# Kernel tuning notes

Measured on AMD Instinct MI355X. Metric: run time of the kernel, lower is better.

The kernel has to match this reference:

```python
import jax, jax.numpy as jnp
import numpy as np

V, D, L, H, T_BLK, DFF = 50257, 768, 12, 12, 1024, 4096
DK = D // H
LN_EPS = 1e-5


def setup_inputs() -> dict:
    key = jax.random.key(0)
    ks = jax.random.split(key, 16)
    s = 0.02
    inp = {
        "idx": jax.random.randint(ks[0], (2, 1024), 0, V),
        "tok_emb": jax.random.normal(ks[1], (V, D), jnp.float32) * s,
        "pos_emb": jax.random.normal(ks[2], (1, T_BLK, D), jnp.float32) * s,
        "ln1_w": jnp.ones((L, D), jnp.float32),
        "ln1_b": jnp.zeros((L, D), jnp.float32),
        "qkv_w": jax.random.normal(ks[3], (L, 3 * D, D), jnp.float32) * s,
        "qkv_b": jnp.zeros((L, 3 * D), jnp.float32),
        "proj_w": jax.random.normal(ks[4], (L, D, D), jnp.float32) * s,
        "proj_b": jnp.zeros((L, D), jnp.float32),
        "ln2_w": jnp.ones((L, D), jnp.float32),
        "ln2_b": jnp.zeros((L, D), jnp.float32),
        "ff1_w": jax.random.normal(ks[5], (L, DFF, D), jnp.float32) * s,
        "ff1_b": jnp.zeros((L, DFF), jnp.float32),
        "ff2_w": jax.random.normal(ks[6], (L, D, DFF), jnp.float32) * s,
        "ff2_b": jnp.zeros((L, D), jnp.float32),
        "lnf_w": jnp.ones((D,), jnp.float32),
        "lnf_b": jnp.zeros((D,), jnp.float32),
        "head_w": jax.random.normal(ks[7], (V, D), jnp.float32) * s,
    }
    return inp


def _layernorm(x, w, b):
    mu = jnp.mean(x, axis=-1, keepdims=True)
    var = jnp.var(x, axis=-1, keepdims=True)
    return (x - mu) * jax.lax.rsqrt(var + LN_EPS) * w + b


def _gpt_forward(idx, tok_emb, pos_emb, ln1_w, ln1_b, qkv_w, qkv_b, proj_w, proj_b,
                 ln2_w, ln2_b, ff1_w, ff1_b, ff2_w, ff2_b, lnf_w, lnf_b, head_w):
    B, T = idx.shape
    x = tok_emb[idx] + pos_emb[:, :T, :]  # [B,T,D]
    mask = jnp.tril(jnp.ones((T, T), bool))  # causal
    scale = 1.0 / np.sqrt(DK)

    def step(x, p):
        l1w, l1b, qw, qb, pw, pb, l2w, l2b, f1w, f1b, f2w, f2b = p
        h = _layernorm(x, l1w, l1b)
        qkv = h @ qw.T + qb  # [B,T,3D]
        q, k, v = jnp.split(qkv, 3, axis=-1)
        q = q.reshape(B, T, H, DK).transpose(0, 2, 1, 3)  # [B,H,T,DK]
        k = k.reshape(B, T, H, DK).transpose(0, 2, 1, 3)
        v = v.reshape(B, T, H, DK).transpose(0, 2, 1, 3)
        att = jnp.einsum('bhtd,bhsd->bhts', q, k) * scale
        att = jnp.where(mask, att, -jnp.inf)
        att = jax.nn.softmax(att, axis=-1)
        y = jnp.einsum('bhts,bhsd->bhtd', att, v)
        y = y.transpose(0, 2, 1, 3).reshape(B, T, D)
        x = x + y @ pw.T + pb
        h2 = _layernorm(x, l2w, l2b)
        ff = jax.nn.gelu(h2 @ f1w.T + f1b, approximate=False) @ f2w.T + f2b
        return x + ff, None

    params = (ln1_w, ln1_b, qkv_w, qkv_b, proj_w, proj_b,
              ln2_w, ln2_b, ff1_w, ff1_b, ff2_w, ff2_b)
    x, _ = jax.lax.scan(step, x, params)
    x = _layernorm(x, lnf_w, lnf_b)
    return x @ head_w.T  # [B,T,V] logits


def reference(idx, tok_emb, pos_emb, ln1_w, ln1_b, qkv_w, qkv_b, proj_w, proj_b,
              ln2_w, ln2_b, ff1_w, ff1_b, ff2_w, ff2_b, lnf_w, lnf_b, head_w):
    return _gpt_forward(idx, tok_emb, pos_emb, ln1_w, ln1_b, qkv_w, qkv_b, proj_w,
                        proj_b, ln2_w, ln2_b, ff1_w, ff1_b, ff2_w, ff2_b,
                        lnf_w, lnf_b, head_w)
```

## Files before the change

kernel.cpp:

```cpp
#include <hip/hip_runtime.h>
#include <hip/hip_bf16.h>
#include <math.h>

#define Dm 768
#define Tt 1024
#define Bb 2
#define Hh 12
#define DFF 4096
#define Ll 12
#define Vv 50257
#define ROWS (Bb*Tt)
#define LN_EPS 1e-5f

typedef unsigned int uint;
typedef unsigned short ushort;
typedef float f32x4 __attribute__((ext_vector_type(4)));
typedef short bf16x8 __attribute__((ext_vector_type(8)));
typedef ushort us8 __attribute__((ext_vector_type(8)));

__device__ __forceinline__ ushort f2bf(float f) {
  uint u = __builtin_bit_cast(uint, f);
  u += 0x7FFFu + ((u >> 16) & 1u);
  return (ushort)(u >> 16);
}

#define GLL(gp, lp)                                                          \
  __builtin_amdgcn_global_load_lds(                                          \
      (const __attribute__((address_space(1))) uint*)(gp),                   \
      (__attribute__((address_space(3))) uint*)(lp), 16, 0, 0)

#define MF(a, b, c) __builtin_amdgcn_mfma_f32_16x16x32_bf16(a, b, c, 0, 0, 0)

__global__ __launch_bounds__(256) void embed_ln(
    const int* __restrict__ idx, const float* __restrict__ tok,
    const float* __restrict__ pos, const float* __restrict__ w,
    const float* __restrict__ b, float* __restrict__ x,
    ushort* __restrict__ out) {
  const int row = blockIdx.x;
  const int t = row & (Tt - 1);
  const int tid = threadIdx.x;
  const float* tsrc = tok + (size_t)idx[row] * Dm;
  const float* psrc = pos + (size_t)t * Dm;
  float v[3];
  float sum = 0.f, sq = 0.f;
#pragma unroll
  for (int i = 0; i < 3; i++) {
    const int d = tid + i * 256;
    v[i] = tsrc[d] + psrc[d];
    x[(size_t)row * Dm + d] = v[i];
    sum += v[i]; sq += v[i] * v[i];
  }
#pragma unroll
  for (int off = 32; off > 0; off >>= 1) {
    sum += __shfl_xor(sum, off);
    sq  += __shfl_xor(sq, off);
  }
  __shared__ float red[8];
  const int wid = tid >> 6, lane = tid & 63;
  if (lane == 0) { red[wid] = sum; red[wid + 4] = sq; }
  __syncthreads();
  sum = red[0] + red[1] + red[2] + red[3];
  sq  = red[4] + red[5] + red[6] + red[7];
  const float mu = sum * (1.f / Dm);
  const float var = sq * (1.f / Dm) - mu * mu;
  const float rstd = rsqrtf(var + LN_EPS);
  ushort* dst = out + (size_t)row * Dm;
#pragma unroll
  for (int i = 0; i < 3; i++) {
    const int d = tid + i * 256;
    dst[d] = f2bf((v[i] - mu) * rstd * w[d] + b[d]);
  }
}

__global__ __launch_bounds__(192) void red_ln(
    const float* __restrict__ part, int nsk, const float* __restrict__ bias,
    float* __restrict__ x, const float* __restrict__ w,
    const float* __restrict__ b, ushort* __restrict__ out) {
  const int row = blockIdx.x;
  const int tid = threadIdx.x;
  const size_t o4 = (size_t)row * 192 + tid;
  float4 xv = ((const float4*)x)[o4];
  const float4 b4 = ((const float4*)bias)[tid];
  xv.x += b4.x; xv.y += b4.y; xv.z += b4.z; xv.w += b4.w;
  for (int k = 0; k < nsk; k++) {
    const float4 p = ((const float4*)part)[(size_t)k * ROWS * 192 + o4];
    xv.x += p.x; xv.y += p.y; xv.z += p.z; xv.w += p.w;
  }
  ((float4*)x)[o4] = xv;
  float sum = xv.x + xv.y + xv.z + xv.w;
  float sq = xv.x * xv.x + xv.y * xv.y + xv.z * xv.z + xv.w * xv.w;
#pragma unroll
  for (int off = 32; off > 0; off >>= 1) {
    sum += __shfl_xor(sum, off);
    sq  += __shfl_xor(sq, off);
  }
  __shared__ float red[6];
  const int wid = tid >> 6, lane = tid & 63;
  if (lane == 0) { red[wid] = sum; red[wid + 3] = sq; }
  __syncthreads();
  sum = red[0] + red[1] + red[2];
  sq  = red[3] + red[4] + red[5];
  const float mu = sum * (1.f / Dm);
  const float var = sq * (1.f / Dm) - mu * mu;
  const float rstd = rsqrtf(var + LN_EPS);
  const float4 w4 = ((const float4*)w)[tid];
  const float4 bb4 = ((const float4*)b)[tid];
  ushort4 o;
  o.x = f2bf((xv.x - mu) * rstd * w4.x + bb4.x);
  o.y = f2bf((xv.y - mu) * rstd * w4.y + bb4.y);
  o.z = f2bf((xv.z - mu) * rstd * w4.z + bb4.z);
  o.w = f2bf((xv.w - mu) * rstd * w4.w + bb4.w);
  ((ushort4*)out)[o4] = o;
}

#define C1 5308416
#define C2 7077888
#define C3 16515072
#define C4 25952256
#define NALL4 35601600

__global__ __launch_bounds__(256) void convert_all(
    const float* __restrict__ q, const float* __restrict__ p,
    const float* __restrict__ f1, const float* __restrict__ f2,
    const float* __restrict__ hd, ushort* __restrict__ wb) {
  const int stride = gridDim.x * 256;
  for (int i = blockIdx.x * 256 + threadIdx.x; i < NALL4; i += stride) {
    const float* s; int j;
    if (i < C1) { s = q; j = i; }
    else if (i < C2) { s = p; j = i - C1; }
    else if (i < C3) { s = f1; j = i - C2; }
    else if (i < C4) { s = f2; j = i - C3; }
    else { s = hd; j = i - C4; }
    const float4 v = ((const float4*)s)[j];
    ushort4 o;
    o.x = f2bf(v.x); o.y = f2bf(v.y); o.z = f2bf(v.z); o.w = f2bf(v.w);
    ((ushort4*)wb)[i] = o;
  }
}

#define EPI_QKV 0
#define EPI_PART 1
#define EPI_BIAS_GELU 2
#define EPI_NONE 3

template <int EPI>
__global__ __launch_bounds__(256) void gemm_mfma(
    const ushort* __restrict__ A, const ushort* __restrict__ B,
    const float* __restrict__ bias, void* __restrict__ Cv,
    void* __restrict__ Cv2, int Kloop, int Kstr, int Nloc, int ldC) {
  __shared__ char lds[32768];
  const int tid = threadIdx.x;
  const int l = tid & 63;
  const int wid = __builtin_amdgcn_readfirstlane(tid >> 6);
  const int wr = wid >> 1, wc = wid & 1;
  const int m0 = blockIdx.y * 128;
  const int n0 = blockIdx.x * 128;
  const int z = (EPI == EPI_PART) ? blockIdx.z : 0;
  if (EPI == EPI_PART) { A += (size_t)z * Kloop; B += (size_t)z * Kloop; }

  const int cperm = (((l & 3) ^ ((l >> 3) & 3)) * 8);
  const ushort* gA = A + (size_t)(m0 + wid * 32 + (l >> 2)) * Kstr + cperm;
  int rB = n0 + wid * 32 + (l >> 2);
  rB = min(rB, Nloc - 1);
  const ushort* gB = B + (size_t)rB * Kstr + cperm;

  const int rdSw = (l & 15) * 64 + (((l >> 4) ^ ((l >> 1) & 3)) * 16);
  const int aRd = wr * 4096 + rdSw;
  const int bRd = 8192 + wc * 4096 + rdSw;

  f32x4 acc[4][4] = {};
  const int nt = Kloop / 32;

  {
    const int lb = wid * 2048;
    GLL(gA, lds + lb);          GLL(gA + 16 * Kstr, lds + lb + 1024);
    GLL(gB, lds + 8192 + lb);   GLL(gB + 16 * Kstr, lds + 8192 + lb + 1024);
  }

  for (int t = 0; t < nt; ++t) {
    __syncthreads();
    if (t + 1 < nt) {
      const int base = ((t + 1) & 1) * 16384;
      const int lb = base + wid * 2048;
      const ushort* a = gA + (t + 1) * 32;
      const ushort* b = gB + (t + 1) * 32;
      GLL(a, lds + lb);         GLL(a + 16 * Kstr, lds + lb + 1024);
      GLL(b, lds + 8192 + lb);  GLL(b + 16 * Kstr, lds + 8192 + lb + 1024);
    }
    const int base = (t & 1) * 16384;
    bf16x8 av[4], bv[4];
#pragma unroll
    for (int i = 0; i < 4; ++i) {
      av[i] = *(const bf16x8*)(lds + base + aRd + i * 1024);
      bv[i] = *(const bf16x8*)(lds + base + bRd + i * 1024);
    }
#pragma unroll
    for (int i = 0; i < 4; ++i)
#pragma unroll
      for (int j = 0; j < 4; ++j)
        acc[i][j] = MF(av[i], bv[j], acc[i][j]);
  }

#pragma unroll
  for (int fm = 0; fm < 4; ++fm) {
    const int row0 = m0 + wr * 64 + fm * 16 + (l >> 4) * 4;
#pragma unroll
    for (int fn = 0; fn < 4; ++fn) {
      const int col = n0 + wc * 64 + fn * 16 + (l & 15);
      if (col >= Nloc) continue;
      float bi = 0.f;
      if (EPI == EPI_QKV || EPI == EPI_BIAS_GELU) bi = bias[col];
      if (EPI == EPI_QKV && col >= 2 * Dm) {
        const int hh = (col - 2 * Dm) >> 6, dd = col & 63;
        const int bI = row0 >> 10, t0 = row0 & (Tt - 1);
        ushort4 o4;
        o4.x = f2bf(acc[fm][fn][0] + bi);
        o4.y = f2bf(acc[fm][fn][1] + bi);
        o4.z = f2bf(acc[fm][fn][2] + bi);
        o4.w = f2bf(acc[fm][fn][3] + bi);
        *(ushort4*)((ushort*)Cv2 +
                    ((size_t)((bI * Hh + hh) * 64 + dd)) * Tt + t0) = o4;
        continue;
      }
#pragma unroll
      for (int r = 0; r < 4; ++r) {
        float v = acc[fm][fn][r] + bi;
        const size_t off = (size_t)(row0 + r) * ldC + col;
        if (EPI == EPI_BIAS_GELU) {
          v = 0.5f * v * (1.f + erff(v * 0.70710678118654752f));
          ((ushort*)Cv)[off] = f2bf(v);
        } else if (EPI == EPI_QKV) {
          ((ushort*)Cv)[off] = f2bf(v);
        } else if (EPI == EPI_PART) {
          ((float*)Cv)[(size_t)z * ROWS * ldC + off] = v;
        } else {
          ((float*)Cv)[off] = v;
        }
      }
    }
  }
}

__global__ __launch_bounds__(512, 2) void gemm_head8(
    const ushort* __restrict__ A, const ushort* __restrict__ B,
    float* __restrict__ C) {
  __shared__ char lds[131072];
  const int tid = threadIdx.x;
  const int l = tid & 63;
  const int wid = __builtin_amdgcn_readfirstlane(tid >> 6);
  const int wm = wid >> 2, wn = wid & 3;
  const int s = l & 15, g = l >> 4;

  const int bid = blockIdx.x;
  const int swz = (bid & 7) * 197 + (bid >> 3);
  const int pan = swz >> 3, mrw = swz & 7;
  const int m0 = mrw * 256;
  const int n0 = pan * 256;

  const int r0 = tid >> 3;
  const int q0 = (tid & 7) ^ (r0 & 7);
  const ushort* pA0 = A + (size_t)(m0 + r0) * Dm + q0 * 8;
  const ushort* pA1 = pA0 + (size_t)64 * Dm;
  const ushort* pB[2][2];
  pB[0][0] = B + (size_t)min(n0 + r0, Vv - 1) * Dm + q0 * 8;
  pB[0][1] = B + (size_t)min(n0 + 64 + r0, Vv - 1) * Dm + q0 * 8;
  pB[1][0] = B + (size_t)min(n0 + 128 + r0, Vv - 1) * Dm + q0 * 8;
  pB[1][1] = B + (size_t)min(n0 + 192 + r0, Vv - 1) * Dm + q0 * 8;

#define STG_A(t, h) do { if ((t) < 12) {                                     \
    char* _d = lds + ((((t) & 1) * 2 + (h)) * 16384);                        \
    GLL(pA0 + (size_t)(h) * 98304 + (t) * 64, _d + tid * 16);                \
    GLL(pA1 + (size_t)(h) * 98304 + (t) * 64, _d + 8192 + tid * 16);         \
  }} while (0)
#define STG_B(t, h) do { if ((t) < 12) {                                     \
    char* _d = lds + 65536 + ((((t) & 1) * 2 + (h)) * 16384);                \
    GLL(pB[h][0] + (t) * 64, _d + tid * 16);                                 \
    GLL(pB[h][1] + (t) * 64, _d + 8192 + tid * 16);                          \
  }} while (0)

  const int aK0 = ((0 * 4 + g) ^ (s & 7)) * 16;
  const int aK1 = ((1 * 4 + g) ^ (s & 7)) * 16;
  const int aBase = wm * 16384 + s * 128;
  const int bBase = 65536 + (wn >> 1) * 16384 + (wn & 1) * 8192 + s * 128;

  f32x4 acc[8][4] = {};
  bf16x8 bv[4][2];

#define PH(t, p, STAGES, VMC)                                                \
  {                                                                          \
    const int cur = ((t) & 1) * 32768;                                       \
    if ((p) == 1) {                                                          \
      _Pragma("unroll")                                                      \
      for (int fn = 0; fn < 4; fn++) {                                       \
        bv[fn][0] = *(const bf16x8*)(lds + cur + bBase + fn * 2048 + aK0);   \
        bv[fn][1] = *(const bf16x8*)(lds + cur + bBase + fn * 2048 + aK1);   \
      }                                                                      \
    }                                                                        \
    bf16x8 a00 = *(const bf16x8*)(lds + cur + aBase + (2*(p)-2)*2048 + aK0); \
    bf16x8 a01 = *(const bf16x8*)(lds + cur + aBase + (2*(p)-2)*2048 + aK1); \
    bf16x8 a10 = *(const bf16x8*)(lds + cur + aBase + (2*(p)-1)*2048 + aK0); \
    bf16x8 a11 = *(const bf16x8*)(lds + cur + aBase + (2*(p)-1)*2048 + aK1); \
    STAGES;                                                                  \
    __builtin_amdgcn_s_barrier();                                            \
    asm volatile("s_waitcnt lgkmcnt(0)" ::: "memory");                       \
    __builtin_amdgcn_sched_barrier(0);                                       \
    __builtin_amdgcn_s_setprio(1);                                           \
    _Pragma("unroll")                                                        \
    for (int fn = 0; fn < 4; fn++) {                                         \
      acc[2*(p)-2][fn] = MF(a00, bv[fn][0], acc[2*(p)-2][fn]);               \
      acc[2*(p)-2][fn] = MF(a01, bv[fn][1], acc[2*(p)-2][fn]);               \
      acc[2*(p)-1][fn] = MF(a10, bv[fn][0], acc[2*(p)-1][fn]);               \
      acc[2*(p)-1][fn] = MF(a11, bv[fn][1], acc[2*(p)-1][fn]);               \
    }                                                                        \
    __builtin_amdgcn_s_setprio(0);                                           \
    VMC;                                                                     \
    __builtin_amdgcn_s_barrier();                                            \
  }

  STG_B(0, 0); STG_B(0, 1); STG_A(0, 0); STG_A(0, 1); STG_B(1, 0); STG_B(1, 1);
  asm volatile("s_waitcnt vmcnt(4)" ::: "memory");
  __builtin_amdgcn_s_barrier();

#pragma unroll 1
  for (int i = 0; i < 6; ++i) {
    const int t0 = 2 * i, t1 = 2 * i + 1, t2 = 2 * i + 2, t3 = 2 * i + 3;
    PH(t0, 1, { STG_A(t1, 0); }, {});
    PH(t0, 2, { STG_A(t1, 1); STG_B(t2, 0); }, {});
    PH(t0, 3, { STG_B(t2, 1); }, {});
    if (i < 5) {
      PH(t0, 4, {}, { asm volatile("s_waitcnt vmcnt(4)" ::: "memory"); });
    } else {
      PH(t0, 4, {}, { asm volatile("s_waitcnt vmcnt(0)" ::: "memory"); });
    }
    PH(t1, 1, { STG_A(t2, 0); }, {});
    PH(t1, 2, { STG_A(t2, 1); }, {});
    PH(t1, 3, { STG_B(t3, 0); }, {});
    if (i < 5) {
      PH(t1, 4, { STG_B(t3, 1); },
         { asm volatile("s_waitcnt vmcnt(4)" ::: "memory"); });
    } else {
      PH(t1, 4, {}, {});
    }
  }

#pragma unroll
  for (int fm = 0; fm < 8; ++fm) {
    const int row0 = m0 + wm * 128 + fm * 16 + g * 4;
#pragma unroll
    for (int fn = 0; fn < 4; ++fn) {
      const int col = n0 + wn * 64 + fn * 16 + s;
      if (col >= Vv) continue;
#pragma unroll
      for (int r = 0; r < 4; ++r)
        C[(size_t)(row0 + r) * Vv + col] = acc[fm][fn][r];
    }
  }
#undef PH
#undef STG_A
#undef STG_B
}

__global__ __launch_bounds__(128) void attn_mfma(
    const ushort* __restrict__ qkv, const ushort* __restrict__ vTg,
    ushort* __restrict__ y) {
  __shared__ char lds[36864];
  const int tid = threadIdx.x;
  const int l = tid & 63;
  const int w = tid >> 6;
  const int s = l & 15, g = l >> 4;
  const int bq = gridDim.x - 1 - blockIdx.x;
  const int h = blockIdx.y, b = blockIdx.z;
  const int bh = b * Hh + h;

  const int qrow = bq * 32 + w * 16 + s;
  const ushort* qp = qkv + (size_t)(b * Tt + qrow) * 2304 + h * 64 + g * 8;
  const bf16x8 aq0 = *(const bf16x8*)qp;
  const bf16x8 aq1 = *(const bf16x8*)(qp + 32);

  size_t gofs[8];
#pragma unroll
  for (int i = 0; i < 8; i++) {
    const int c = tid + i * 128;
    if (i < 4) {
      const int kr = c >> 3;
      gofs[i] = (size_t)(b * Tt + kr) * 2304 + Dm + h * 64 + ((c & 7) ^ (kr & 7)) * 8;
    } else {
      const int cv = c - 512;
      const int vr = cv >> 3;
      gofs[i] = (size_t)(bh * 64 + vr) * Tt + ((cv & 7) ^ (vr & 7)) * 8;
    }
  }

#define ASTAGE(kt, base)                                                     \
  do {                                                                       \
    _Pragma("unroll")                                                        \
    for (int i = 0; i < 8; i++) {                                            \
      const ushort* p = (i < 4) ? (qkv + gofs[i] + (size_t)(kt) * 147456)    \
                                : (vTg + gofs[i] + (kt) * 64);               \
      GLL(p, lds + (base) + tid * 16 + i * 2048);                            \
    }                                                                        \
  } while (0)

  f32x4 oc[4] = {};
  float mrun[4], lrun[4];
#pragma unroll
  for (int r = 0; r < 4; r++) { mrun[r] = -INFINITY; lrun[r] = 0.f; }

  const int pB = 32768 + w * 2048;
  const int kSw = (s & 7);
  const int nkt = (bq >> 1) + 1;

  ASTAGE(0, 0);
  for (int kt = 0; kt < nkt; ++kt) {
    __syncthreads();
    if (kt + 1 < nkt) ASTAGE(kt + 1, ((kt + 1) & 1) * 16384);
    const int cur = (kt & 1) * 16384;

    f32x4 sc[4];
    __builtin_amdgcn_s_setprio(1);
#pragma unroll
    for (int jn = 0; jn < 4; jn++) {
      const int krow = cur + (jn * 16 + s) * 128;
      const bf16x8 bk0 = *(const bf16x8*)(lds + krow + ((g ^ kSw) * 16));
      const bf16x8 bk1 = *(const bf16x8*)(lds + krow + (((4 + g) ^ kSw) * 16));
      f32x4 z = {};
      z = MF(aq0, bk0, z);
      z = MF(aq1, bk1, z);
      sc[jn] = z;
    }
    __builtin_amdgcn_s_setprio(0);

    float cr[4];
    const bool diag = (kt == nkt - 1);
#pragma unroll
    for (int r = 0; r < 4; r++) {
      const int rowg = bq * 32 + w * 16 + g * 4 + r;
      float v[4];
#pragma unroll
      for (int jn = 0; jn < 4; jn++) {
        v[jn] = sc[jn][r] * 0.125f;
        if (diag && (kt * 64 + jn * 16 + s) > rowg) v[jn] = -INFINITY;
      }
      float mx = fmaxf(fmaxf(v[0], v[1]), fmaxf(v[2], v[3]));
      mx = fmaxf(mx, __shfl_xor(mx, 1));
      mx = fmaxf(mx, __shfl_xor(mx, 2));
      mx = fmaxf(mx, __shfl_xor(mx, 4));
      mx = fmaxf(mx, __shfl_xor(mx, 8));
      const float mnew = fmaxf(mrun[r], mx);
      const float corr = __expf(mrun[r] - mnew);
      mrun[r] = mnew;
      float ps = 0.f;
#pragma unroll
      for (int jn = 0; jn < 4; jn++) {
        const float p = __expf(v[jn] - mnew);
        ps += p;
        *(ushort*)(lds + pB + (g * 4 + r) * 128 +
                   (((2 * jn + (s >> 3)) ^ g) * 16) + (s & 7) * 2) = f2bf(p);
      }
      ps += __shfl_xor(ps, 1);
      ps += __shfl_xor(ps, 2);
      ps += __shfl_xor(ps, 4);
      ps += __shfl_xor(ps, 8);
      lrun[r] = lrun[r] * corr + ps;
      cr[r] = corr;
    }

    const float c01 = (s & 1) ? cr[1] : cr[0];
    const float c23 = (s & 1) ? cr[3] : cr[2];
    const float csel = (s & 2) ? c23 : c01;
    const float ccol = __shfl(csel, ((s >> 2) << 4) | s);
#pragma unroll
    for (int fm = 0; fm < 4; fm++) {
      oc[fm][0] *= ccol; oc[fm][1] *= ccol;
      oc[fm][2] *= ccol; oc[fm][3] *= ccol;
    }

    const bf16x8 bp0 = *(const bf16x8*)(lds + pB + s * 128 + ((g ^ (s >> 2)) * 16));
    const bf16x8 bp1 = *(const bf16x8*)(lds + pB + s * 128 + (((4 + g) ^ (s >> 2)) * 16));
    __builtin_amdgcn_s_setprio(1);
#pragma unroll
    for (int fm = 0; fm < 4; fm++) {
      const int vrow = cur + 8192 + (fm * 16 + s) * 128;
      const bf16x8 av0 = *(const bf16x8*)(lds + vrow + ((g ^ kSw) * 16));
      const bf16x8 av1 = *(const bf16x8*)(lds + vrow + (((4 + g) ^ kSw) * 16));
      oc[fm] = MF(av0, bp0, oc[fm]);
      oc[fm] = MF(av1, bp1, oc[fm]);
    }
    __builtin_amdgcn_s_setprio(0);
  }

  float li[4];
#pragma unroll
  for (int r = 0; r < 4; r++) li[r] = 1.f / lrun[r];
  const float l01 = (s & 1) ? li[1] : li[0];
  const float l23 = (s & 1) ? li[3] : li[2];
  const float lsel = (s & 2) ? l23 : l01;
  const float lcol = __shfl(lsel, ((s >> 2) << 4) | s);
  ushort* yp = y + (size_t)(b * Tt + qrow) * Dm + h * 64;
#pragma unroll
  for (int fm = 0; fm < 4; fm++) {
    ushort4 o4;
    o4.x = f2bf(oc[fm][0] * lcol);
    o4.y = f2bf(oc[fm][1] * lcol);
    o4.z = f2bf(oc[fm][2] * lcol);
    o4.w = f2bf(oc[fm][3] * lcol);
    *(ushort4*)(yp + fm * 16 + g * 4) = o4;
  }
}

extern "C" void kernel_launch(void* const* d_in, const int* in_sizes, int n_in,
                              void* d_out, int out_size, void* d_ws, size_t ws_size,
                              hipStream_t stream) {
  const int* idx = (const int*)d_in[0];
  const float* tok = (const float*)d_in[1];
  const float* pos = (const float*)d_in[2];
  const float* ln1w = (const float*)d_in[3];
  const float* ln1b = (const float*)d_in[4];
  const float* qkvw = (const float*)d_in[5];
  const float* qkvb = (const float*)d_in[6];
  const float* projw = (const float*)d_in[7];
  const float* projb = (const float*)d_in[8];
  const float* ln2w = (const float*)d_in[9];
  const float* ln2b = (const float*)d_in[10];
  const float* ff1w = (const float*)d_in[11];
  const float* ff1b = (const float*)d_in[12];
  const float* ff2w = (const float*)d_in[13];
  const float* ff2b = (const float*)d_in[14];
  const float* lnfw = (const float*)d_in[15];
  const float* lnfb = (const float*)d_in[16];
  const float* headw = (const float*)d_in[17];
  float* out = (float*)d_out;

  char* ws = (char*)d_ws;
  ushort* h    = (ushort*)ws;
  float*  x    = (float*)(ws + 3145728);
  ushort* y    = (ushort*)(ws + 9437184);
  ushort* qkv  = (ushort*)(ws + 12582912);
  ushort* vTg  = (ushort*)(ws + 22020096);
  ushort* ff   = (ushort*)(ws + 25165824);
  ushort* wb   = (ushort*)(ws + 41943040);
  float* projPart = (float*)(ws + 326755840);
  float* ff2Part  = (float*)(ws + 351921664);

  const size_t oPROJ = (size_t)Ll * 3 * Dm * Dm;
  const size_t oFF1  = oPROJ + (size_t)Ll * Dm * Dm;
  const size_t oFF2  = oFF1 + (size_t)Ll * DFF * Dm;
  const size_t oHEAD = oFF2 + (size_t)Ll * Dm * DFF;

  convert_all<<<4096, 256, 0, stream>>>(qkvw, projw, ff1w, ff2w, headw, wb);

  embed_ln<<<ROWS, 256, 0, stream>>>(idx, tok, pos, ln1w, ln1b, x, h);

  for (int l = 0; l < Ll; l++) {
    gemm_mfma<EPI_QKV><<<dim3(18, 16), 256, 0, stream>>>(
        h, wb + (size_t)l * 3 * Dm * Dm, qkvb + l * 3 * Dm, qkv, vTg,
        Dm, Dm, 3 * Dm, 3 * Dm);
    attn_mfma<<<dim3(32, Hh, Bb), 128, 0, stream>>>(qkv, vTg, y);
    gemm_mfma<EPI_PART><<<dim3(6, 16, 4), 256, 0, stream>>>(
        y, wb + oPROJ + (size_t)l * Dm * Dm, nullptr, projPart, nullptr,
        Dm / 4, Dm, Dm, Dm);
    red_ln<<<ROWS, 192, 0, stream>>>(projPart, 4, projb + l * Dm, x,
                                     ln2w + l * Dm, ln2b + l * Dm, h);
    gemm_mfma<EPI_BIAS_GELU><<<dim3(32, 16), 256, 0, stream>>>(
        h, wb + oFF1 + (size_t)l * DFF * Dm, ff1b + l * DFF, ff, nullptr,
        Dm, Dm, DFF, DFF);
    gemm_mfma<EPI_PART><<<dim3(6, 16, 4), 256, 0, stream>>>(
        ff, wb + oFF2 + (size_t)l * Dm * DFF, nullptr, ff2Part, nullptr,
        DFF / 4, DFF, Dm, Dm);
    const float* nw = (l == Ll - 1) ? lnfw : ln1w + (l + 1) * Dm;
    const float* nb = (l == Ll - 1) ? lnfb : ln1b + (l + 1) * Dm;
    red_ln<<<ROWS, 192, 0, stream>>>(ff2Part, 4, ff2b + l * Dm, x, nw, nb, h);
  }

  gemm_head8<<<1576, 512, 0, stream>>>(h, wb + oHEAD, out);
}
```

Before: 2.055 ms.

## Replace head GEMM with smaller 256x128 tile and simple double-buffered pipeline

The LM-head GEMM moves from a 256x256 tile with a hand-scheduled multi-phase K=64 pipeline and 128KB of LDS to a 256x128 tile. The new loop steps K=32 per iteration over a plain two-stage double buffer in 48KB of LDS, and launch bounds are raised to 4 blocks per CU for higher occupancy. The grid doubles to 3144 blocks. In exchange, operand reuse per tile drops, B traffic from global memory rises, each K step pays a __syncthreads, and the fine-grained interleaving of loads with MFMA is lost.

```diff
diff --git a/kernel.cpp b/kernel.cpp
--- a/kernel.cpp
+++ b/kernel.cpp
@@ -241,10 +241,10 @@
   }
 }
 
-__global__ __launch_bounds__(512, 2) void gemm_head8(
+__global__ __launch_bounds__(512, 4) void gemm_head2(
     const ushort* __restrict__ A, const ushort* __restrict__ B,
     float* __restrict__ C) {
-  __shared__ char lds[131072];
+  __shared__ char lds[49152];
   const int tid = threadIdx.x;
   const int l = tid & 63;
   const int wid = __builtin_amdgcn_readfirstlane(tid >> 6);
@@ -252,112 +252,73 @@
   const int s = l & 15, g = l >> 4;
 
   const int bid = blockIdx.x;
-  const int swz = (bid & 7) * 197 + (bid >> 3);
+  const int swz = (bid & 7) * 393 + (bid >> 3);
   const int pan = swz >> 3, mrw = swz & 7;
   const int m0 = mrw * 256;
-  const int n0 = pan * 256;
-
-  const int r0 = tid >> 3;
-  const int q0 = (tid & 7) ^ (r0 & 7);
-  const ushort* pA0 = A + (size_t)(m0 + r0) * Dm + q0 * 8;
-  const ushort* pA1 = pA0 + (size_t)64 * Dm;
-  const ushort* pB[2][2];
-  pB[0][0] = B + (size_t)min(n0 + r0, Vv - 1) * Dm + q0 * 8;
-  pB[0][1] = B + (size_t)min(n0 + 64 + r0, Vv - 1) * Dm + q0 * 8;
-  pB[1][0] = B + (size_t)min(n0 + 128 + r0, Vv - 1) * Dm + q0 * 8;
-  pB[1][1] = B + (size_t)min(n0 + 192 + r0, Vv - 1) * Dm + q0 * 8;
-
-#define STG_A(t, h) do { if ((t) < 12) {                                     \
-    char* _d = lds + ((((t) & 1) * 2 + (h)) * 16384);                        \
-    GLL(pA0 + (size_t)(h) * 98304 + (t) * 64, _d + tid * 16);                \
-    GLL(pA1 + (size_t)(h) * 98304 + (t) * 64, _d + 8192 + tid * 16);         \
-  }} while (0)
-#define STG_B(t, h) do { if ((t) < 12) {                                     \
-    char* _d = lds + 65536 + ((((t) & 1) * 2 + (h)) * 16384);                \
-    GLL(pB[h][0] + (t) * 64, _d + tid * 16);                                 \
-    GLL(pB[h][1] + (t) * 64, _d + 8192 + tid * 16);                          \
-  }} while (0)
-
-  const int aK0 = ((0 * 4 + g) ^ (s & 7)) * 16;
-  const int aK1 = ((1 * 4 + g) ^ (s & 7)) * 16;
-  const int aBase = wm * 16384 + s * 128;
-  const int bBase = 65536 + (wn >> 1) * 16384 + (wn & 1) * 8192 + s * 128;
-
-  f32x4 acc[8][4] = {};
-  bf16x8 bv[4][2];
-
-#define PH(t, p, STAGES, VMC)                                                \
-  {                                                                          \
-    const int cur = ((t) & 1) * 32768;                                       \
-    if ((p) == 1) {                                                          \
-      _Pragma("unroll")                                                      \
-      for (int fn = 0; fn < 4; fn++) {                                       \
-        bv[fn][0] = *(const bf16x8*)(lds + cur + bBase + fn * 2048 + aK0);   \
-        bv[fn][1] = *(const bf16x8*)(lds + cur + bBase + fn * 2048 + aK1);   \
-      }                                                                      \
-    }                                                                        \
-    bf16x8 a00 = *(const bf16x8*)(lds + cur + aBase + (2*(p)-2)*2048 + aK0); \
-    bf16x8 a01 = *(const bf16x8*)(lds + cur + aBase + (2*(p)-2)*2048 + aK1); \
-    bf16x8 a10 = *(const bf16x8*)(lds + cur + aBase + (2*(p)-1)*2048 + aK0); \
-    bf16x8 a11 = *(const bf16x8*)(lds + cur + aBase + (2*(p)-1)*2048 + aK1); \
-    STAGES;                                                                  \
-    __builtin_amdgcn_s_barrier();                                            \
-    asm volatile("s_waitcnt lgkmcnt(0)" ::: "memory");                       \
-    __builtin_amdgcn_sched_barrier(0);                                       \
-    __builtin_amdgcn_s_setprio(1);                                           \
-    _Pragma("unroll")                                                        \
-    for (int fn = 0; fn < 4; fn++) {                                         \
-      acc[2*(p)-2][fn] = MF(a00, bv[fn][0], acc[2*(p)-2][fn]);               \
-      acc[2*(p)-2][fn] = MF(a01, bv[fn][1], acc[2*(p)-2][fn]);               \
-      acc[2*(p)-1][fn] = MF(a10, bv[fn][0], acc[2*(p)-1][fn]);               \
-      acc[2*(p)-1][fn] = MF(a11, bv[fn][1], acc[2*(p)-1][fn]);               \
-    }                                                                        \
-    __builtin_amdgcn_s_setprio(0);                                           \
-    VMC;                                                                     \
-    __builtin_amdgcn_s_barrier();                                            \
-  }
-
-  STG_B(0, 0); STG_B(0, 1); STG_A(0, 0); STG_A(0, 1); STG_B(1, 0); STG_B(1, 1);
-  asm volatile("s_waitcnt vmcnt(4)" ::: "memory");
-  __builtin_amdgcn_s_barrier();
-
+  const int n0 = pan * 128;
+
+  const int rA0 = tid >> 2, qA0 = (tid & 3) ^ ((rA0 >> 1) & 3);
+  const int rA1 = (tid + 512) >> 2, qA1 = (tid & 3) ^ ((rA1 >> 1) & 3);
+  const ushort* gA0 = A + (size_t)(m0 + rA0) * Dm + qA0 * 8;
+  const ushort* gA1 = A + (size_t)(m0 + rA1) * Dm + qA1 * 8;
+  int rBg = n0 + (tid >> 2);
+  rBg = min(rBg, Vv - 1);
+  const ushort* gB = B + (size_t)rBg * Dm + (((tid & 3) ^ (((tid >> 2) >> 1) & 3)) * 8);
+
+#define HSTG(t, base)                                                        \
+  do {                                                                       \
+    GLL(gA0 + (t) * 32, lds + (base) + tid * 16);                            \
+    GLL(gA1 + (t) * 32, lds + (base) + 8192 + tid * 16);                     \
+    GLL(gB + (t) * 32, lds + (base) + 16384 + tid * 16);                     \
+  } while (0)
+
+  int aOff[8], bOff[2];
+#pragma unroll
+  for (int fm = 0; fm < 8; fm++) {
+    const int r = wm * 128 + fm * 16 + s;
+    aOff[fm] = r * 64 + ((g ^ ((r >> 1) & 3)) * 16);
+  }
+#pragma unroll
+  for (int fn = 0; fn < 2; fn++) {
+    const int r = wn * 32 + fn * 16 + s;
+    bOff[fn] = 16384 + r * 64 + ((g ^ ((r >> 1) & 3)) * 16);
+  }
+
+  f32x4 acc[8][2] = {};
+
+  HSTG(0, 0);
 #pragma unroll 1
-  for (int i = 0; i < 6; ++i) {
-    const int t0 = 2 * i, t1 = 2 * i + 1, t2 = 2 * i + 2, t3 = 2 * i + 3;
-    PH(t0, 1, { STG_A(t1, 0); }, {});
-    PH(t0, 2, { STG_A(t1, 1); STG_B(t2, 0); }, {});
-    PH(t0, 3, { STG_B(t2, 1); }, {});
-    if (i < 5) {
-      PH(t0, 4, {}, { asm volatile("s_waitcnt vmcnt(4)" ::: "memory"); });
-    } else {
-      PH(t0, 4, {}, { asm volatile("s_waitcnt vmcnt(0)" ::: "memory"); });
-    }
-    PH(t1, 1, { STG_A(t2, 0); }, {});
-    PH(t1, 2, { STG_A(t2, 1); }, {});
-    PH(t1, 3, { STG_B(t3, 0); }, {});
-    if (i < 5) {
-      PH(t1, 4, { STG_B(t3, 1); },
-         { asm volatile("s_waitcnt vmcnt(4)" ::: "memory"); });
-    } else {
-      PH(t1, 4, {}, {});
-    }
+  for (int t = 0; t < 24; ++t) {
+    __syncthreads();
+    if (t + 1 < 24) HSTG(t + 1, ((t + 1) & 1) * 24576);
+    const int base = (t & 1) * 24576;
+    bf16x8 av[8], bv[2];
+#pragma unroll
+    for (int fm = 0; fm < 8; fm++) av[fm] = *(const bf16x8*)(lds + base + aOff[fm]);
+#pragma unroll
+    for (int fn = 0; fn < 2; fn++) bv[fn] = *(const bf16x8*)(lds + base + bOff[fn]);
+    __builtin_amdgcn_s_setprio(1);
+#pragma unroll
+    for (int fm = 0; fm < 8; fm++)
+#pragma unroll
+      for (int fn = 0; fn < 2; fn++)
+        acc[fm][fn] = MF(av[fm], bv[fn], acc[fm][fn]);
+    __builtin_amdgcn_s_setprio(0);
   }
 
 #pragma unroll
   for (int fm = 0; fm < 8; ++fm) {
     const int row0 = m0 + wm * 128 + fm * 16 + g * 4;
 #pragma unroll
-    for (int fn = 0; fn < 4; ++fn) {
-      const int col = n0 + wn * 64 + fn * 16 + s;
+    for (int fn = 0; fn < 2; ++fn) {
+      const int col = n0 + wn * 32 + fn * 16 + s;
       if (col >= Vv) continue;
 #pragma unroll
       for (int r = 0; r < 4; ++r)
         C[(size_t)(row0 + r) * Vv + col] = acc[fm][fn][r];
     }
   }
-#undef PH
-#undef STG_A
-#undef STG_B
+#undef HSTG
 }
 
 __global__ __launch_bounds__(128) void attn_mfma(
@@ -572,5 +533,5 @@
     red_ln<<<ROWS, 192, 0, stream>>>(ff2Part, 4, ff2b + l * Dm, x, nw, nb, h);
   }
 
-  gemm_head8<<<1576, 512, 0, stream>>>(h, wb + oHEAD, out);
-}
+  gemm_head2<<<3144, 512, 0, stream>>>(h, wb + oHEAD, out);
+}
```

After: 2.076 ms. About the same (+1.0%).

## Deepen K-tile to 64 in per-layer MFMA GEMM with new swizzled LDS layout

Applied to the files above, without the earlier changes.

The per-layer bf16 MFMA GEMM now stages 64-wide K slices instead of 32, doubling LDS to 64KB with double buffering. Global-to-LDS loads are redistributed across all threads with an XOR row swizzle, and each K-tile runs two MFMA sub-steps. This halves the number of barriers and loop iterations per GEMM and gives more work between syncs. The cost is higher LDS use per block, which may lower occupancy.

```diff
diff --git a/kernel.cpp b/kernel.cpp
--- a/kernel.cpp
+++ b/kernel.cpp
@@ -148,7 +148,7 @@
     const ushort* __restrict__ A, const ushort* __restrict__ B,
     const float* __restrict__ bias, void* __restrict__ Cv,
     void* __restrict__ Cv2, int Kloop, int Kstr, int Nloc, int ldC) {
-  __shared__ char lds[32768];
+  __shared__ char lds[65536];
   const int tid = threadIdx.x;
   const int l = tid & 63;
   const int wid = __builtin_amdgcn_readfirstlane(tid >> 6);
@@ -158,47 +158,59 @@
   const int z = (EPI == EPI_PART) ? blockIdx.z : 0;
   if (EPI == EPI_PART) { A += (size_t)z * Kloop; B += (size_t)z * Kloop; }
 
-  const int cperm = (((l & 3) ^ ((l >> 3) & 3)) * 8);
-  const ushort* gA = A + (size_t)(m0 + wid * 32 + (l >> 2)) * Kstr + cperm;
-  int rB = n0 + wid * 32 + (l >> 2);
-  rB = min(rB, Nloc - 1);
-  const ushort* gB = B + (size_t)rB * Kstr + cperm;
-
-  const int rdSw = (l & 15) * 64 + (((l >> 4) ^ ((l >> 1) & 3)) * 16);
-  const int aRd = wr * 4096 + rdSw;
-  const int bRd = 8192 + wc * 4096 + rdSw;
+  const ushort* gA[4];
+  const ushort* gB[4];
+#pragma unroll
+  for (int j = 0; j < 4; j++) {
+    const int c = tid + j * 256;
+    const int r = c >> 3;
+    const int q = (c & 7) ^ (r & 7);
+    gA[j] = A + (size_t)(m0 + r) * Kstr + q * 8;
+    const int rb = min(n0 + r, Nloc - 1);
+    gB[j] = B + (size_t)rb * Kstr + q * 8;
+  }
+
+#define LSTG(t, base)                                                        \
+  do {                                                                       \
+    _Pragma("unroll")                                                        \
+    for (int j = 0; j < 4; j++) {                                            \
+      GLL(gA[j] + (t) * 64, lds + (base) + (tid + j * 256) * 16);            \
+      GLL(gB[j] + (t) * 64, lds + (base) + 16384 + (tid + j * 256) * 16);    \
+    }                                                                        \
+  } while (0)
+
+  const int s = l & 15, g = l >> 4;
+  int aRd[4], bRd[4], cOf[2];
+#pragma unroll
+  for (int i = 0; i < 4; i++) {
+    aRd[i] = (wr * 64 + i * 16 + s) * 128;
+    bRd[i] = 16384 + (wc * 64 + i * 16 + s) * 128;
+  }
+  cOf[0] = ((g + 0) ^ (s & 7)) * 16;
+  cOf[1] = ((g + 4) ^ (s & 7)) * 16;
 
   f32x4 acc[4][4] = {};
-  const int nt = Kloop / 32;
-
-  {
-    const int lb = wid * 2048;
-    GLL(gA, lds + lb);          GLL(gA + 16 * Kstr, lds + lb + 1024);
-    GLL(gB, lds + 8192 + lb);   GLL(gB + 16 * Kstr, lds + 8192 + lb + 1024);
-  }
-
+  const int nt = Kloop / 64;
+
+  LSTG(0, 0);
   for (int t = 0; t < nt; ++t) {
     __syncthreads();
-    if (t + 1 < nt) {
-      const int base = ((t + 1) & 1) * 16384;
-      const int lb = base + wid * 2048;
-      const ushort* a = gA + (t + 1) * 32;
-      const ushort* b = gB + (t + 1) * 32;
-      GLL(a, lds + lb);         GLL(a + 16 * Kstr, lds + lb + 1024);
-      GLL(b, lds + 8192 + lb);  GLL(b + 16 * Kstr, lds + 8192 + lb + 1024);
-    }
-    const int base = (t & 1) * 16384;
-    bf16x8 av[4], bv[4];
-#pragma unroll
-    for (int i = 0; i < 4; ++i) {
-      av[i] = *(const bf16x8*)(lds + base + aRd + i * 1024);
-      bv[i] = *(const bf16x8*)(lds + base + bRd + i * 1024);
-    }
-#pragma unroll
-    for (int i = 0; i < 4; ++i)
-#pragma unroll
-      for (int j = 0; j < 4; ++j)
-        acc[i][j] = MF(av[i], bv[j], acc[i][j]);
+    if (t + 1 < nt) LSTG(t + 1, ((t + 1) & 1) * 32768);
+    const int base = (t & 1) * 32768;
+#pragma unroll
+    for (int ks = 0; ks < 2; ++ks) {
+      bf16x8 av[4], bv[4];
+#pragma unroll
+      for (int i = 0; i < 4; ++i) {
+        av[i] = *(const bf16x8*)(lds + base + aRd[i] + cOf[ks]);
+        bv[i] = *(const bf16x8*)(lds + base + bRd[i] + cOf[ks]);
+      }
+#pragma unroll
+      for (int i = 0; i < 4; ++i)
+#pragma unroll
+        for (int j = 0; j < 4; ++j)
+          acc[i][j] = MF(av[i], bv[j], acc[i][j]);
+    }
   }
 
 #pragma unroll
@@ -239,6 +251,7 @@
       }
     }
   }
+#undef LSTG
 }
 
 __global__ __launch_bounds__(512, 2) void gemm_head8(
```

After: 1.957 ms. 4.7% less time.
